# Kernel tuning notes

Measured on AMD Instinct MI355X. Metric: run time of the kernel, lower is better.

## Reference

```python
import jax, jax.numpy as jnp
import numpy as np

NUM_HEADS = 16
HEAD_DIM = 64
NEG_INF = -1000000000.0


def rotary_embedding(x, seq_len, head_dim):
    # x: (batch, seq, heads, head_dim)
    positions = jnp.arange(seq_len)
    dim_pairs = jnp.arange(0, head_dim, 2)
    freqs = 1.0 / 10000.0 ** (dim_pairs / head_dim)
    angles = positions[:, None] * freqs[None, :]          # (seq, head_dim/2)
    cos = jnp.cos(angles)[:, None, :]                     # (seq, 1, head_dim/2) -> broadcast over heads
    sin = jnp.sin(angles)[:, None, :]
    x1 = x[..., ::2]
    x2 = x[..., 1::2]
    out1 = x1 * cos - x2 * sin
    out2 = x1 * sin + x2 * cos
    return jnp.stack([out1, out2], axis=-1).reshape(x.shape)


def setup_inputs() -> dict:
    key = jax.random.key(0)
    k1, k2, k3 = jax.random.split(key, 3)
    batch, seq_len, embed_dim = 2, 2048, 1024
    x = jax.random.normal(k1, (batch, seq_len, embed_dim), dtype=jnp.float32)
    W_qkv = jax.random.normal(k2, (embed_dim, 3 * NUM_HEADS * HEAD_DIM), dtype=jnp.float32) * 0.02
    W_out = jax.random.normal(k3, (NUM_HEADS * HEAD_DIM, embed_dim), dtype=jnp.float32) * 0.02
    return {"x": x, "W_qkv": W_qkv, "W_out": W_out}


def reference(x, W_qkv, W_out):
    batch, seq_len, embed_dim = x.shape
    qkv = jnp.einsum('bse,ef->bsf', x, W_qkv)
    qkv = qkv.reshape(batch, seq_len, 3, NUM_HEADS, HEAD_DIM)
    q, k, v = qkv[:, :, 0], qkv[:, :, 1], qkv[:, :, 2]
    q = rotary_embedding(q, seq_len, HEAD_DIM)
    k = rotary_embedding(k, seq_len, HEAD_DIM)
    scale = 1.0 / jnp.sqrt(jnp.asarray(HEAD_DIM, dtype=x.dtype))
    scores = jnp.einsum('bqhd,bkhd->bhqk', q, k) * scale   # (B,H,S,S)
    mask = jnp.tril(jnp.ones((seq_len, seq_len), dtype=bool))[None, None, :, :]
    scores = jnp.where(mask, scores, NEG_INF)
    weights = jax.nn.softmax(scores, axis=-1)
    out = jnp.einsum('bhqk,bkhd->bqhd', weights, v)
    out = out.reshape(batch, seq_len, NUM_HEADS * HEAD_DIM)
    return jnp.einsum('bsf,fe->bse', out, W_out)
```

## Files before the change

kernel.cpp:

```cpp
#include <hip/hip_runtime.h>
#include <hip/hip_bf16.h>

typedef __attribute__((ext_vector_type(8))) short short8;
typedef __attribute__((ext_vector_type(4))) float float4v;

__global__ __launch_bounds__(256) void cvt_f32_bf16(
    const float* __restrict__ in, __hip_bfloat16* __restrict__ out, int n4) {
  const int i = blockIdx.x * 256 + threadIdx.x;
  if (i >= n4) return;
  const float4 v = *(const float4*)(in + (size_t)i * 4);
  __hip_bfloat16 o[4];
  o[0] = __float2bfloat16(v.x); o[1] = __float2bfloat16(v.y);
  o[2] = __float2bfloat16(v.z); o[3] = __float2bfloat16(v.w);
  *(uint2*)(out + (size_t)i * 4) = *(const uint2*)o;
}

__global__ __launch_bounds__(256) void transpose_f32_bf16(
    const float* __restrict__ in, __hip_bfloat16* __restrict__ out,
    int R, int C) {
  __shared__ __hip_bfloat16 tile[32][33];
  const int c0 = blockIdx.x * 32, r0 = blockIdx.y * 32;
  const int tx = threadIdx.x & 31, ty = threadIdx.x >> 5;
  #pragma unroll
  for (int i = ty; i < 32; i += 8)
    tile[i][tx] = __float2bfloat16(in[(size_t)(r0 + i) * C + (c0 + tx)]);
  __syncthreads();
  #pragma unroll
  for (int i = ty; i < 32; i += 8)
    out[(size_t)(c0 + i) * R + (r0 + tx)] = tile[tx][i];
}

template <typename OutT>
__global__ __launch_bounds__(256) void gemm_bt(
    const __hip_bfloat16* __restrict__ A,
    const __hip_bfloat16* __restrict__ Bt,
    OutT* __restrict__ C,
    int M, int N, int K) {
  __shared__ __hip_bfloat16 lA[128][64];
  __shared__ __hip_bfloat16 lB[128][64];
  const int t = threadIdx.x;
  const int lane = t & 63, wave = t >> 6;
  const int quad = lane >> 4, ln = lane & 15;
  const int m0 = blockIdx.y * 128, n0 = blockIdx.x * 128;
  const int wm = (wave >> 1) * 64, wn = (wave & 1) * 64;
  const int srow = lane >> 3;
  const int schunk = ((lane & 7) ^ srow) * 8;

  float4v acc[4][4];
  #pragma unroll
  for (int i = 0; i < 4; ++i)
    #pragma unroll
    for (int j = 0; j < 4; ++j)
      acc[i][j] = (float4v){0.f, 0.f, 0.f, 0.f};

  for (int kt = 0; kt < K; kt += 64) {
    __syncthreads();
    #pragma unroll
    for (int q = 0; q < 4; ++q) {
      const int rbase = wave * 32 + q * 8;
      __builtin_amdgcn_global_load_lds(
          (const __attribute__((address_space(1))) void*)
              (A + (size_t)(m0 + rbase + srow) * K + kt + schunk),
          (__attribute__((address_space(3))) void*)&lA[rbase][0], 16, 0, 0);
      __builtin_amdgcn_global_load_lds(
          (const __attribute__((address_space(1))) void*)
              (Bt + (size_t)(n0 + rbase + srow) * K + kt + schunk),
          (__attribute__((address_space(3))) void*)&lB[rbase][0], 16, 0, 0);
    }
    __syncthreads();
    #pragma unroll
    for (int step = 0; step < 2; ++step) {
      short8 af[4], bf[4];
      #pragma unroll
      for (int i = 0; i < 4; ++i)
        af[i] = *(const short8*)&lA[wm + i * 16 + ln][((step * 4 + quad) ^ (ln & 7)) * 8];
      #pragma unroll
      for (int j = 0; j < 4; ++j)
        bf[j] = *(const short8*)&lB[wn + j * 16 + ln][((step * 4 + quad) ^ (ln & 7)) * 8];
      #pragma unroll
      for (int i = 0; i < 4; ++i)
        #pragma unroll
        for (int j = 0; j < 4; ++j)
          acc[i][j] = __builtin_amdgcn_mfma_f32_16x16x32_bf16(af[i], bf[j], acc[i][j], 0, 0, 0);
    }
  }
  #pragma unroll
  for (int i = 0; i < 4; ++i)
    #pragma unroll
    for (int j = 0; j < 4; ++j)
      #pragma unroll
      for (int r = 0; r < 4; ++r) {
        const int row = m0 + wm + i * 16 + quad * 4 + r;
        const int col = n0 + wn + j * 16 + ln;
        if constexpr (__is_same(OutT, float))
          C[(size_t)row * N + col] = acc[i][j][r];
        else
          C[(size_t)row * N + col] = __float2bfloat16(acc[i][j][r]);
      }
}

__global__ __launch_bounds__(512) void rope_reshape(
    const __hip_bfloat16* __restrict__ qkv,
    __hip_bfloat16* __restrict__ Q,
    __hip_bfloat16* __restrict__ K) {
  const int row = blockIdx.x;
  const int s = row & 2047;
  const int b = row >> 11;
  const int t = threadIdx.x;
  const int h = t >> 5, pr = t & 31;
  const int d0 = pr * 2;
  const float freq = powf(10000.f, -(float)d0 / 64.f);
  const float ang = (float)s * freq;
  float sn, cs;
  sincosf(ang, &sn, &cs);

  const size_t in_base = (size_t)row * 3072;
  const size_t o = (((size_t)(b * 16 + h)) * 2048 + s) * 64 + d0;

  __hip_bfloat162 q2 = *(const __hip_bfloat162*)&qkv[in_base + h * 64 + d0];
  float x1 = __bfloat162float(q2.x), x2 = __bfloat162float(q2.y);
  __hip_bfloat162 qo;
  qo.x = __float2bfloat16((x1 * cs - x2 * sn) * 0.125f);
  qo.y = __float2bfloat16((x1 * sn + x2 * cs) * 0.125f);
  *(__hip_bfloat162*)&Q[o] = qo;

  __hip_bfloat162 k2 = *(const __hip_bfloat162*)&qkv[in_base + 1024 + h * 64 + d0];
  x1 = __bfloat162float(k2.x); x2 = __bfloat162float(k2.y);
  __hip_bfloat162 ko;
  ko.x = __float2bfloat16(x1 * cs - x2 * sn);
  ko.y = __float2bfloat16(x1 * sn + x2 * cs);
  *(__hip_bfloat162*)&K[o] = ko;
}

__global__ __launch_bounds__(256) void v_transpose(
    const __hip_bfloat16* __restrict__ qkv,
    __hip_bfloat16* __restrict__ Vt) {
  __shared__ __hip_bfloat16 tile[64][65];
  const int bh = blockIdx.y;
  const int h = bh & 15, b = bh >> 4;
  const int s0 = blockIdx.x * 64;
  const int tx = threadIdx.x & 63, ty = threadIdx.x >> 6;
  #pragma unroll
  for (int i = ty; i < 64; i += 4)
    tile[i][tx] = qkv[(size_t)(b * 2048 + s0 + i) * 3072 + 2048 + h * 64 + tx];
  __syncthreads();
  #pragma unroll
  for (int i = ty; i < 64; i += 4)
    Vt[((size_t)bh * 64 + i) * 2048 + s0 + tx] = tile[tx][i];
}

__global__ __launch_bounds__(256) void attention(
    const __hip_bfloat16* __restrict__ Q,
    const __hip_bfloat16* __restrict__ K,
    const __hip_bfloat16* __restrict__ Vt,
    __hip_bfloat16* __restrict__ attn) {
  __shared__ __hip_bfloat16 lK[2][64][64];
  __shared__ __hip_bfloat16 lV[2][64][64];
  __shared__ __hip_bfloat16 lP[4][16][72];
  const int t = threadIdx.x;
  const int lane = t & 63, w = t >> 6;
  const int quad = lane >> 4, ln = lane & 15;
  const int bh = blockIdx.x;
  const int pair = blockIdx.y;
  const size_t base = (size_t)bh * 2048 * 64;
  const __hip_bfloat16* Qb = Q + base;
  const __hip_bfloat16* Kb = K + base;
  const __hip_bfloat16* Vb = Vt + base;
  const int b = bh >> 4, h = bh & 15;

  short8 ones;
  #pragma unroll
  for (int i = 0; i < 8; ++i) ones[i] = (short)0x3F80;

  const int srow = lane >> 3;
  const int schunk = ((lane & 7) ^ srow) * 8;
  const int rb0 = w * 16;

  #pragma unroll
  for (int ph = 0; ph < 2; ++ph) {
    const int qt = (ph == 0) ? pair : 31 - pair;
    const int q0 = qt * 64;

    __syncthreads();

    #pragma unroll
    for (int g = 0; g < 2; ++g) {
      const int rbase = rb0 + g * 8;
      __builtin_amdgcn_global_load_lds(
          (const __attribute__((address_space(1))) void*)
              (Kb + (size_t)(rbase + srow) * 64 + schunk),
          (__attribute__((address_space(3))) void*)&lK[0][rbase][0], 16, 0, 0);
      __builtin_amdgcn_global_load_lds(
          (const __attribute__((address_space(1))) void*)
              (Vb + (size_t)(rbase + srow) * 2048 + schunk),
          (__attribute__((address_space(3))) void*)&lV[0][rbase][0], 16, 0, 0);
    }

    short8 qf[2];
    {
      const size_t qrow = (size_t)(q0 + w * 16 + ln) * 64;
      qf[0] = *(const short8*)(Qb + qrow + quad * 8);
      qf[1] = *(const short8*)(Qb + qrow + 32 + quad * 8);
    }

    float4v acc_o[4];
    #pragma unroll
    for (int dt = 0; dt < 4; ++dt) acc_o[dt] = (float4v){0.f, 0.f, 0.f, 0.f};
    float4v acc_l = (float4v){0.f, 0.f, 0.f, 0.f};

    for (int kt = 0; kt <= qt; ++kt) {
      const int buf = kt & 1;
      __syncthreads();

      if (kt < qt) {
        #pragma unroll
        for (int g = 0; g < 2; ++g) {
          const int rbase = rb0 + g * 8;
          __builtin_amdgcn_global_load_lds(
              (const __attribute__((address_space(1))) void*)
                  (Kb + (size_t)((kt + 1) * 64 + rbase + srow) * 64 + schunk),
              (__attribute__((address_space(3))) void*)&lK[buf ^ 1][rbase][0], 16, 0, 0);
          __builtin_amdgcn_global_load_lds(
              (const __attribute__((address_space(1))) void*)
                  (Vb + (size_t)(rbase + srow) * 2048 + (kt + 1) * 64 + schunk),
              (__attribute__((address_space(3))) void*)&lV[buf ^ 1][rbase][0], 16, 0, 0);
        }
      }

      float4v s4[4];
      #pragma unroll
      for (int nt = 0; nt < 4; ++nt) {
        float4v a = (float4v){0.f, 0.f, 0.f, 0.f};
        #pragma unroll
        for (int step = 0; step < 2; ++step) {
          short8 kf = *(const short8*)&lK[buf][nt * 16 + ln][((step * 4 + quad) ^ (ln & 7)) * 8];
          a = __builtin_amdgcn_mfma_f32_16x16x32_bf16(qf[step], kf, a, 0, 0, 0);
        }
        s4[nt] = a;
      }
      if (kt == qt) {
        #pragma unroll
        for (int nt = 0; nt < 4; ++nt)
          #pragma unroll
          for (int r = 0; r < 4; ++r) {
            const int sk = kt * 64 + nt * 16 + ln;
            const int qr = q0 + w * 16 + quad * 4 + r;
            if (sk > qr) s4[nt][r] = -64.f;
          }
      }
      #pragma unroll
      for (int nt = 0; nt < 4; ++nt)
        #pragma unroll
        for (int r = 0; r < 4; ++r)
          lP[w][quad * 4 + r][nt * 16 + ln] = __float2bfloat16(__expf(s4[nt][r]));
      #pragma unroll
      for (int step = 0; step < 2; ++step) {
        short8 pf = *(const short8*)&lP[w][ln][step * 32 + quad * 8];
        acc_l = __builtin_amdgcn_mfma_f32_16x16x32_bf16(pf, ones, acc_l, 0, 0, 0);
        #pragma unroll
        for (int dt = 0; dt < 4; ++dt) {
          short8 vf = *(const short8*)&lV[buf][dt * 16 + ln][((step * 4 + quad) ^ (ln & 7)) * 8];
          acc_o[dt] = __builtin_amdgcn_mfma_f32_16x16x32_bf16(pf, vf, acc_o[dt], 0, 0, 0);
        }
      }
    }

    float inv_l[4];
    #pragma unroll
    for (int r = 0; r < 4; ++r) inv_l[r] = 1.0f / acc_l[r];
    #pragma unroll
    for (int dt = 0; dt < 4; ++dt)
      #pragma unroll
      for (int r = 0; r < 4; ++r) {
        const int qr = q0 + w * 16 + quad * 4 + r;
        const size_t rg = (size_t)(b * 2048 + qr);
        const int col = h * 64 + dt * 16 + ln;
        attn[rg * 1024 + col] = __float2bfloat16(acc_o[dt][r] * inv_l[r]);
      }
  }
}

extern "C" void kernel_launch(void* const* d_in, const int* in_sizes, int n_in,
                              void* d_out, int out_size, void* d_ws, size_t ws_size,
                              hipStream_t stream) {
  const float* x    = (const float*)d_in[0];
  const float* Wqkv = (const float*)d_in[1];
  const float* Wout = (const float*)d_in[2];
  float* out = (float*)d_out;

  __hip_bfloat16* ws = (__hip_bfloat16*)d_ws;
  __hip_bfloat16* xb    = ws;
  __hip_bfloat16* WqkvT = xb    + (size_t)4096 * 1024;
  __hip_bfloat16* WoutT = WqkvT + (size_t)3072 * 1024;
  __hip_bfloat16* qkv   = WoutT + (size_t)1024 * 1024;
  __hip_bfloat16* Q     = qkv   + (size_t)4096 * 3072;
  __hip_bfloat16* K     = Q     + (size_t)32 * 2048 * 64;
  __hip_bfloat16* Vt    = K     + (size_t)32 * 2048 * 64;
  __hip_bfloat16* attn  = Vt    + (size_t)32 * 2048 * 64;

  cvt_f32_bf16<<<4096, 256, 0, stream>>>(x, xb, 4096 * 1024 / 4);
  transpose_f32_bf16<<<dim3(3072 / 32, 1024 / 32), 256, 0, stream>>>(Wqkv, WqkvT, 1024, 3072);
  transpose_f32_bf16<<<dim3(1024 / 32, 1024 / 32), 256, 0, stream>>>(Wout, WoutT, 1024, 1024);
  gemm_bt<__hip_bfloat16><<<dim3(3072 / 128, 4096 / 128), 256, 0, stream>>>(xb, WqkvT, qkv, 4096, 3072, 1024);
  rope_reshape<<<4096, 512, 0, stream>>>(qkv, Q, K);
  v_transpose<<<dim3(32, 32), 256, 0, stream>>>(qkv, Vt);
  attention<<<dim3(32, 16), 256, 0, stream>>>(Q, K, Vt, attn);
  gemm_bt<float><<<dim3(1024 / 128, 4096 / 128), 256, 0, stream>>>(attn, WoutT, out, 4096, 1024, 1024);
}
```

Before: 199.4 us.

## Keep attention probabilities in registers via transposed QK^T and fp16 PV MFMA

```diff
diff --git a/kernel.cpp b/kernel.cpp
--- a/kernel.cpp
+++ b/kernel.cpp
@@ -3,6 +3,8 @@
 
 typedef __attribute__((ext_vector_type(8))) short short8;
 typedef __attribute__((ext_vector_type(4))) float float4v;
+typedef __attribute__((ext_vector_type(4))) _Float16 half4;
+typedef __attribute__((ext_vector_type(2))) __fp16 fp16x2;
 
 __global__ __launch_bounds__(256) void cvt_f32_bf16(
     const float* __restrict__ in, __hip_bfloat16* __restrict__ out, int n4) {
@@ -113,6 +115,7 @@
   const float ang = (float)s * freq;
   float sn, cs;
   sincosf(ang, &sn, &cs);
+  const float qs = 0.125f * 1.44269504088896340736f;
 
   const size_t in_base = (size_t)row * 3072;
   const size_t o = (((size_t)(b * 16 + h)) * 2048 + s) * 64 + d0;
@@ -120,8 +123,8 @@
   __hip_bfloat162 q2 = *(const __hip_bfloat162*)&qkv[in_base + h * 64 + d0];
   float x1 = __bfloat162float(q2.x), x2 = __bfloat162float(q2.y);
   __hip_bfloat162 qo;
-  qo.x = __float2bfloat16((x1 * cs - x2 * sn) * 0.125f);
-  qo.y = __float2bfloat16((x1 * sn + x2 * cs) * 0.125f);
+  qo.x = __float2bfloat16((x1 * cs - x2 * sn) * qs);
+  qo.y = __float2bfloat16((x1 * sn + x2 * cs) * qs);
   *(__hip_bfloat162*)&Q[o] = qo;
 
   __hip_bfloat162 k2 = *(const __hip_bfloat162*)&qkv[in_base + 1024 + h * 64 + d0];
@@ -134,15 +137,16 @@
 
 __global__ __launch_bounds__(256) void v_transpose(
     const __hip_bfloat16* __restrict__ qkv,
-    __hip_bfloat16* __restrict__ Vt) {
-  __shared__ __hip_bfloat16 tile[64][65];
+    _Float16* __restrict__ Vt) {
+  __shared__ _Float16 tile[64][65];
   const int bh = blockIdx.y;
   const int h = bh & 15, b = bh >> 4;
   const int s0 = blockIdx.x * 64;
   const int tx = threadIdx.x & 63, ty = threadIdx.x >> 6;
   #pragma unroll
   for (int i = ty; i < 64; i += 4)
-    tile[i][tx] = qkv[(size_t)(b * 2048 + s0 + i) * 3072 + 2048 + h * 64 + tx];
+    tile[i][tx] = (_Float16)__bfloat162float(
+        qkv[(size_t)(b * 2048 + s0 + i) * 3072 + 2048 + h * 64 + tx]);
   __syncthreads();
   #pragma unroll
   for (int i = ty; i < 64; i += 4)
@@ -152,11 +156,10 @@
 __global__ __launch_bounds__(256) void attention(
     const __hip_bfloat16* __restrict__ Q,
     const __hip_bfloat16* __restrict__ K,
-    const __hip_bfloat16* __restrict__ Vt,
+    const _Float16* __restrict__ Vt,
     __hip_bfloat16* __restrict__ attn) {
   __shared__ __hip_bfloat16 lK[2][64][64];
-  __shared__ __hip_bfloat16 lV[2][64][64];
-  __shared__ __hip_bfloat16 lP[4][16][72];
+  __shared__ _Float16       lV[2][64][64];
   const int t = threadIdx.x;
   const int lane = t & 63, w = t >> 6;
   const int quad = lane >> 4, ln = lane & 15;
@@ -165,12 +168,12 @@
   const size_t base = (size_t)bh * 2048 * 64;
   const __hip_bfloat16* Qb = Q + base;
   const __hip_bfloat16* Kb = K + base;
-  const __hip_bfloat16* Vb = Vt + base;
+  const _Float16* Vb = Vt + base;
   const int b = bh >> 4, h = bh & 15;
 
-  short8 ones;
-  #pragma unroll
-  for (int i = 0; i < 8; ++i) ones[i] = (short)0x3F80;
+  half4 vones;
+  #pragma unroll
+  for (int i = 0; i < 4; ++i) vones[i] = (_Float16)1.0f;
 
   const int srow = lane >> 3;
   const int schunk = ((lane & 7) ^ srow) * 8;
@@ -234,7 +237,7 @@
         #pragma unroll
         for (int step = 0; step < 2; ++step) {
           short8 kf = *(const short8*)&lK[buf][nt * 16 + ln][((step * 4 + quad) ^ (ln & 7)) * 8];
-          a = __builtin_amdgcn_mfma_f32_16x16x32_bf16(qf[step], kf, a, 0, 0, 0);
+          a = __builtin_amdgcn_mfma_f32_16x16x32_bf16(kf, qf[step], a, 0, 0, 0);
         }
         s4[nt] = a;
       }
@@ -243,40 +246,42 @@
         for (int nt = 0; nt < 4; ++nt)
           #pragma unroll
           for (int r = 0; r < 4; ++r) {
-            const int sk = kt * 64 + nt * 16 + ln;
-            const int qr = q0 + w * 16 + quad * 4 + r;
+            const int sk = kt * 64 + nt * 16 + quad * 4 + r;
+            const int qr = q0 + w * 16 + ln;
             if (sk > qr) s4[nt][r] = -64.f;
           }
       }
-      #pragma unroll
-      for (int nt = 0; nt < 4; ++nt)
-        #pragma unroll
-        for (int r = 0; r < 4; ++r)
-          lP[w][quad * 4 + r][nt * 16 + ln] = __float2bfloat16(__expf(s4[nt][r]));
-      #pragma unroll
-      for (int step = 0; step < 2; ++step) {
-        short8 pf = *(const short8*)&lP[w][ln][step * 32 + quad * 8];
-        acc_l = __builtin_amdgcn_mfma_f32_16x16x32_bf16(pf, ones, acc_l, 0, 0, 0);
+      half4 pf[4];
+      #pragma unroll
+      for (int nt = 0; nt < 4; ++nt) {
+        const fp16x2 lo = __builtin_amdgcn_cvt_pkrtz(exp2f(s4[nt][0]), exp2f(s4[nt][1]));
+        const fp16x2 hi = __builtin_amdgcn_cvt_pkrtz(exp2f(s4[nt][2]), exp2f(s4[nt][3]));
+        pf[nt][0] = (_Float16)lo[0]; pf[nt][1] = (_Float16)lo[1];
+        pf[nt][2] = (_Float16)hi[0]; pf[nt][3] = (_Float16)hi[1];
+      }
+      #pragma unroll
+      for (int s = 0; s < 4; ++s) {
+        acc_l = __builtin_amdgcn_mfma_f32_16x16x16f16(vones, pf[s], acc_l, 0, 0, 0);
         #pragma unroll
         for (int dt = 0; dt < 4; ++dt) {
-          short8 vf = *(const short8*)&lV[buf][dt * 16 + ln][((step * 4 + quad) ^ (ln & 7)) * 8];
-          acc_o[dt] = __builtin_amdgcn_mfma_f32_16x16x32_bf16(pf, vf, acc_o[dt], 0, 0, 0);
+          half4 vf = *(const half4*)&lV[buf][dt * 16 + ln]
+              [((s * 2 + (quad >> 1)) ^ (ln & 7)) * 8 + (quad & 1) * 4];
+          acc_o[dt] = __builtin_amdgcn_mfma_f32_16x16x16f16(vf, pf[s], acc_o[dt], 0, 0, 0);
         }
       }
     }
 
-    float inv_l[4];
-    #pragma unroll
-    for (int r = 0; r < 4; ++r) inv_l[r] = 1.0f / acc_l[r];
-    #pragma unroll
-    for (int dt = 0; dt < 4; ++dt)
-      #pragma unroll
-      for (int r = 0; r < 4; ++r) {
-        const int qr = q0 + w * 16 + quad * 4 + r;
-        const size_t rg = (size_t)(b * 2048 + qr);
-        const int col = h * 64 + dt * 16 + ln;
-        attn[rg * 1024 + col] = __float2bfloat16(acc_o[dt][r] * inv_l[r]);
-      }
+    const float inv_l = 1.0f / acc_l[0];
+    const int qr = q0 + w * 16 + ln;
+    const size_t rg = (size_t)(b * 2048 + qr) * 1024 + h * 64;
+    #pragma unroll
+    for (int dt = 0; dt < 4; ++dt) {
+      __hip_bfloat16 o4[4];
+      #pragma unroll
+      for (int r = 0; r < 4; ++r)
+        o4[r] = __float2bfloat16(acc_o[dt][r] * inv_l);
+      *(uint2*)&attn[rg + dt * 16 + quad * 4] = *(const uint2*)o4;
+    }
   }
 }
 
@@ -295,8 +300,8 @@
   __hip_bfloat16* qkv   = WoutT + (size_t)1024 * 1024;
   __hip_bfloat16* Q     = qkv   + (size_t)4096 * 3072;
   __hip_bfloat16* K     = Q     + (size_t)32 * 2048 * 64;
-  __hip_bfloat16* Vt    = K     + (size_t)32 * 2048 * 64;
-  __hip_bfloat16* attn  = Vt    + (size_t)32 * 2048 * 64;
+  _Float16*       Vt    = (_Float16*)(K + (size_t)32 * 2048 * 64);
+  __hip_bfloat16* attn  = (__hip_bfloat16*)(Vt + (size_t)32 * 2048 * 64);
 
   cvt_f32_bf16<<<4096, 256, 0, stream>>>(x, xb, 4096 * 1024 / 4);
   transpose_f32_bf16<<<dim3(3072 / 32, 1024 / 32), 256, 0, stream>>>(Wqkv, WqkvT, 1024, 3072);
```

Measured after the change: 200.9 us. Within noise of the previous version (+0.7%).
